# Optimization experiments

Measured on AMD Instinct MI355X. Metric: run time of the kernel, lower is better.

## Reference

```python
import jax, jax.numpy as jnp
import numpy as np

NUM_EXPERTS = 16
HIDDEN_DIM = 1024
TOP_K = 4
INPUT_DIM = 4096
OUTPUT_DIM = 4096
BATCH = 4096


def setup_inputs() -> dict:
    key = jax.random.key(0)
    ks = jax.random.split(key, 6)
    total_cols = NUM_EXPERTS * HIDDEN_DIM
    return {
        "x": jax.random.normal(ks[0], (BATCH, INPUT_DIM), dtype=jnp.float32),
        "gate_w": jax.random.normal(ks[1], (INPUT_DIM, NUM_EXPERTS), dtype=jnp.float32) * 0.02,
        "gate_b": jnp.zeros((NUM_EXPERTS,), dtype=jnp.float32),
        "weight": jax.random.normal(ks[2], (INPUT_DIM, total_cols), dtype=jnp.float32) * 0.01,
        "agg_w": jax.random.normal(ks[3], (total_cols, OUTPUT_DIM), dtype=jnp.float32) * 0.02,
        "agg_b": jnp.zeros((OUTPUT_DIM,), dtype=jnp.float32),
    }


def reference(x, gate_w, gate_b, weight, agg_w, agg_b):
    # 1) gating logits (batch, E), 2) sum over batch -> (E,)
    gating_logits = x @ gate_w + gate_b
    gating_sum = gating_logits.sum(axis=0)
    # 3) global top-k expert selection -> binary mask over experts
    _, topk_inds = jax.lax.top_k(gating_sum, TOP_K)
    expert_mask = jnp.zeros((NUM_EXPERTS,), dtype=x.dtype).at[topk_inds].set(1.0)
    # 4/5) block-sparse matmul: mask replicated over all row blocks, so each
    # expert's column block [e*H:(e+1)*H] is x @ W_block if selected else 0.
    out_sparse = x @ weight  # (batch, E*H)
    col_mask = jnp.repeat(expert_mask, HIDDEN_DIM)  # (E*H,)
    out_sparse = out_sparse * col_mask[None, :]
    # 6) aggregator
    final_out = out_sparse @ agg_w + agg_b
    return final_out
```

## Files before the change

kernel.cpp:

```cpp
#include <hip/hip_runtime.h>
#include <hip/hip_bf16.h>


#define BATCH 4096
#define DIN 4096
#define DOUTD 4096
#define NE 16
#define HD 1024
#define TOPK 4
#define TOTC (NE * HD)
#define NT 64

using bf16 = __hip_bfloat16;
typedef __attribute__((ext_vector_type(8))) short short8;
typedef __attribute__((ext_vector_type(4))) float f32x4;

__device__ inline short f2bs(float f) {
  __hip_bfloat16 h = __float2bfloat16(f);
  return *reinterpret_cast<short*>(&h);
}

__global__ void k_pcol(const float* __restrict__ x, float* __restrict__ pcol) {
  int c = blockIdx.x * 256 + threadIdx.x;
  int r0 = blockIdx.y * 128;
  float s = 0.f;
  for (int r = r0; r < r0 + 128; ++r) s += x[(size_t)r * DIN + c];
  pcol[(size_t)blockIdx.y * DIN + c] = s;
}

__global__ void k_red(const float* __restrict__ pcol, float* __restrict__ colsum) {
  int c = blockIdx.x * 256 + threadIdx.x;
  float s = 0.f;
  for (int j = 0; j < 32; ++j) s += pcol[(size_t)j * DIN + c];
  colsum[c] = s;
}

__global__ void k_gate(const float* __restrict__ colsum, const float* __restrict__ gw,
                       const float* __restrict__ gb, int* __restrict__ ids) {
  __shared__ float red[4][16];
  __shared__ float gs[16];
  int t = threadIdx.x;
  int e = t & 15, kg = t >> 4;
  float p = 0.f;
  for (int k = kg; k < DIN; k += 16) p += colsum[k] * gw[(size_t)k * NE + e];
  p += __shfl_down(p, 32);
  p += __shfl_down(p, 16);
  if ((t & 63) < 16) red[t >> 6][e] = p;
  __syncthreads();
  if (t < 16) gs[t] = red[0][t] + red[1][t] + red[2][t] + red[3][t] + (float)BATCH * gb[t];
  __syncthreads();
  if (t == 0) {
    float v[16];
    #pragma unroll
    for (int i = 0; i < 16; ++i) v[i] = gs[i];
    for (int j = 0; j < TOPK; ++j) {
      int bi = 0;
      float bv = v[0];
      for (int i2 = 1; i2 < 16; ++i2) {
        if (v[i2] > bv) { bv = v[i2]; bi = i2; }
      }
      ids[j] = bi;
      v[bi] = -3.4e38f;
    }
  }
}

__global__ void k_cvt_x(const float* __restrict__ x, bf16* __restrict__ xb) {
  size_t i = ((size_t)blockIdx.x * 256 + threadIdx.x) * 8;
  float4 v0 = *reinterpret_cast<const float4*>(x + i);
  float4 v1 = *reinterpret_cast<const float4*>(x + i + 4);
  short8 r;
  r[0] = f2bs(v0.x); r[1] = f2bs(v0.y); r[2] = f2bs(v0.z); r[3] = f2bs(v0.w);
  r[4] = f2bs(v1.x); r[5] = f2bs(v1.y); r[6] = f2bs(v1.z); r[7] = f2bs(v1.w);
  *reinterpret_cast<short8*>(reinterpret_cast<char*>(xb) + i * 2) = r;
}

__global__ void k_gather_w(const float* __restrict__ w, const int* __restrict__ ids,
                           bf16* __restrict__ wbt) {
  __shared__ float tile[32][33];
  int bid = blockIdx.x;
  int k0 = (bid & 127) * 32, n0 = (bid >> 7) * 32;
  int t = threadIdx.x;
  int tx = t & 31, ty = t >> 5;
  int e = ids[n0 >> 10];
  size_t wcol = (size_t)e * HD + (n0 & 1023) + tx;
  #pragma unroll
  for (int j = 0; j < 4; ++j) {
    int k = k0 + ty + j * 8;
    tile[ty + j * 8][tx] = w[(size_t)k * TOTC + wcol];
  }
  __syncthreads();
  #pragma unroll
  for (int j = 0; j < 4; ++j) {
    int n = n0 + ty + j * 8;
    wbt[(size_t)n * DIN + k0 + tx] = __float2bfloat16(tile[tx][ty + j * 8]);
  }
}

__global__ void k_gather_a(const float* __restrict__ a, const int* __restrict__ ids,
                           bf16* __restrict__ abt) {
  __shared__ float tile[32][33];
  int bid = blockIdx.x;
  int k0 = (bid & 127) * 32, n0 = (bid >> 7) * 32;
  int t = threadIdx.x;
  int tx = t & 31, ty = t >> 5;
  int e = ids[k0 >> 10];
  #pragma unroll
  for (int j = 0; j < 4; ++j) {
    int k = k0 + ty + j * 8;
    size_t ar = (size_t)e * HD + (k & 1023);
    tile[ty + j * 8][tx] = a[ar * DOUTD + n0 + tx];
  }
  __syncthreads();
  #pragma unroll
  for (int j = 0; j < 4; ++j) {
    int n = n0 + ty + j * 8;
    abt[(size_t)n * DIN + k0 + tx] = __float2bfloat16(tile[tx][ty + j * 8]);
  }
}

#define MFMA_BF16 __builtin_amdgcn_mfma_f32_16x16x32_bf16

#define MFMA16(MF0)                                                             \
  __builtin_amdgcn_s_setprio(1);                                               \
  _Pragma("unroll") for (int nf = 0; nf < 4; ++nf) {                            \
    acc[MF0][nf] = MFMA_BF16(aA0, bfrag[nf][0], acc[MF0][nf], 0, 0, 0);         \
    acc[MF0][nf] = MFMA_BF16(aA1, bfrag[nf][1], acc[MF0][nf], 0, 0, 0);         \
    acc[MF0 + 1][nf] = MFMA_BF16(aB0, bfrag[nf][0], acc[MF0 + 1][nf], 0, 0, 0); \
    acc[MF0 + 1][nf] = MFMA_BF16(aB1, bfrag[nf][1], acc[MF0 + 1][nf], 0, 0, 0); \
  }                                                                             \
  __builtin_amdgcn_s_setprio(0);

template <int STORE_F32>
__global__ __launch_bounds__(512, 2) void k_gemm8(
    const bf16* __restrict__ A, const bf16* __restrict__ Bt,
    bf16* __restrict__ Cb, float* __restrict__ Cf, const float* __restrict__ bias) {
  __shared__ __align__(16) char smraw[131072];
  const int t = threadIdx.x;
  const int lane = t & 63;
  const int w = t >> 6;
  const int wr = w >> 2;
  const int wc = w & 3;

  const int bid = blockIdx.x;
  const int swz = (bid & 7) * 32 + (bid >> 3);
  const int bm = (swz >> 4) * 256;
  const int bn = (swz & 15) * 256;

  f32x4 acc[8][4] = {};
  short8 bfrag[4][2];

  const int srow = w * 16 + (lane >> 3);
  const int sgr = lane & 7;

  auto STAGE_A = [&](int buf, int half, int kt) {
    char* lb = smraw + buf * 65536 + half * 16384 + w * 2048 + lane * 16;
    #pragma unroll
    for (int i = 0; i < 2; ++i) {
      int r = srow + i * 8;
      const bf16* g = A + (size_t)(bm + half * 128 + r) * 4096 + kt * 64 + ((sgr ^ (r & 7)) * 8);
      __builtin_amdgcn_global_load_lds(
          (const __attribute__((address_space(1))) void*)g,
          (__attribute__((address_space(3))) void*)(lb + i * 1024), 16, 0, 0);
    }
  };
  auto STAGE_B = [&](int buf, int half, int kt) {
    char* lb = smraw + buf * 65536 + 32768 + half * 16384 + w * 2048 + lane * 16;
    #pragma unroll
    for (int i = 0; i < 2; ++i) {
      int r = srow + i * 8;
      const bf16* g = Bt + (size_t)(bn + half * 128 + r) * 4096 + kt * 64 + ((sgr ^ (r & 7)) * 8);
      __builtin_amdgcn_global_load_lds(
          (const __attribute__((address_space(1))) void*)g,
          (__attribute__((address_space(3))) void*)(lb + i * 1024), 16, 0, 0);
    }
  };
  auto LDA = [&](int buf, int mf, int kk) -> short8 {
    int r = mf * 16 + (lane & 15);
    int kb = ((kk * 4 + (lane >> 4)) ^ (r & 7)) * 16;
    return *reinterpret_cast<const short8*>(smraw + buf * 65536 + wr * 16384 + r * 128 + kb);
  };
  auto LDB = [&](int buf, int nf, int kk) -> short8 {
    int nc = wc * 64 + nf * 16 + (lane & 15);
    int half = nc >> 7, r = nc & 127;
    int kb = ((kk * 4 + (lane >> 4)) ^ (r & 7)) * 16;
    return *reinterpret_cast<const short8*>(smraw + buf * 65536 + 32768 + half * 16384 + r * 128 + kb);
  };

  STAGE_B(0, 0, 0); STAGE_B(0, 1, 0);
  STAGE_A(0, 0, 0); STAGE_A(0, 1, 0);
  STAGE_B(1, 0, 1); STAGE_B(1, 1, 1);
  asm volatile("s_waitcnt vmcnt(4)" ::: "memory");
  __builtin_amdgcn_s_barrier();

  for (int j = 0; j < NT; ++j) {
    const int cur = j & 1, nxt = cur ^ 1;
    {
      #pragma unroll
      for (int nf = 0; nf < 4; ++nf) {
        bfrag[nf][0] = LDB(cur, nf, 0);
        bfrag[nf][1] = LDB(cur, nf, 1);
      }
      short8 aA0 = LDA(cur, 0, 0), aA1 = LDA(cur, 0, 1);
      short8 aB0 = LDA(cur, 1, 0), aB1 = LDA(cur, 1, 1);
      if (j + 1 < NT) STAGE_A(nxt, 0, j + 1);
      __builtin_amdgcn_s_barrier();
      MFMA16(0)
      __builtin_amdgcn_s_barrier();
    }
    {
      short8 aA0 = LDA(cur, 2, 0), aA1 = LDA(cur, 2, 1);
      short8 aB0 = LDA(cur, 3, 0), aB1 = LDA(cur, 3, 1);
      if (j + 1 < NT) STAGE_A(nxt, 1, j + 1);
      __builtin_amdgcn_s_barrier();
      MFMA16(2)
      __builtin_amdgcn_s_barrier();
    }
    {
      short8 aA0 = LDA(cur, 4, 0), aA1 = LDA(cur, 4, 1);
      short8 aB0 = LDA(cur, 5, 0), aB1 = LDA(cur, 5, 1);
      if (j + 2 < NT) STAGE_B(cur, 0, j + 2);
      __builtin_amdgcn_s_barrier();
      MFMA16(4)
      __builtin_amdgcn_s_barrier();
    }
    {
      short8 aA0 = LDA(cur, 6, 0), aA1 = LDA(cur, 6, 1);
      short8 aB0 = LDA(cur, 7, 0), aB1 = LDA(cur, 7, 1);
      if (j + 2 < NT) STAGE_B(cur, 1, j + 2);
      if (j < NT - 2) {
        asm volatile("s_waitcnt vmcnt(4)" ::: "memory");
      } else {
        asm volatile("s_waitcnt vmcnt(0)" ::: "memory");
      }
      __builtin_amdgcn_s_barrier();
      MFMA16(6)
      __builtin_amdgcn_s_barrier();
    }
  }

  const int cr = (lane >> 4) * 4;
  const int cc = lane & 15;
  #pragma unroll
  for (int mf = 0; mf < 8; ++mf) {
    #pragma unroll
    for (int nf = 0; nf < 4; ++nf) {
      int row = bm + wr * 128 + mf * 16 + cr;
      int col = bn + wc * 64 + nf * 16 + cc;
      #pragma unroll
      for (int r = 0; r < 4; ++r) {
        if constexpr (STORE_F32) {
          Cf[(size_t)(row + r) * 4096 + col] = acc[mf][nf][r] + bias[col];
        } else {
          Cb[(size_t)(row + r) * 4096 + col] = __float2bfloat16(acc[mf][nf][r]);
        }
      }
    }
  }
}

extern "C" void kernel_launch(void* const* d_in, const int* in_sizes, int n_in,
                              void* d_out, int out_size, void* d_ws, size_t ws_size,
                              hipStream_t stream) {
  const float* x = (const float*)d_in[0];
  const float* gate_w = (const float*)d_in[1];
  const float* gate_b = (const float*)d_in[2];
  const float* weight = (const float*)d_in[3];
  const float* agg_w = (const float*)d_in[4];
  const float* agg_b = (const float*)d_in[5];
  float* out = (float*)d_out;
  char* ws = (char*)d_ws;

  float* pcol = (float*)ws;
  float* colsum = (float*)(ws + 524288);
  int* ids = (int*)(ws + 540672);
  bf16* mid = (bf16*)(ws + (1u << 20));
  bf16* abt = (bf16*)(ws + (1u << 20) + (32u << 20));
  bf16* xb = (bf16*)d_out;
  bf16* wbt = (bf16*)((char*)d_out + (32u << 20));

  k_pcol<<<dim3(16, 32), 256, 0, stream>>>(x, pcol);
  k_red<<<16, 256, 0, stream>>>(pcol, colsum);
  k_gate<<<1, 256, 0, stream>>>(colsum, gate_w, gate_b, ids);
  k_cvt_x<<<8192, 256, 0, stream>>>(x, xb);
  k_gather_w<<<16384, 256, 0, stream>>>(weight, ids, wbt);
  k_gemm8<0><<<256, 512, 0, stream>>>(xb, wbt, mid, nullptr, nullptr);
  k_gather_a<<<16384, 256, 0, stream>>>(agg_w, ids, abt);
  k_gemm8<1><<<256, 512, 0, stream>>>(mid, abt, nullptr, out, agg_b);
}
```

Before: 410.6 us.

## Fuse x bf16 conversion with column sums, widen gather tiles, unroll GEMM loop

Merges the x-to-bf16 conversion into the column-sum kernel so x is read once, using float4 loads and four partial rows per block. The weight and aggregator gather-transpose kernels move to 64x64 tiles with float4 loads and 16-byte bf16 stores, which cuts the block count and the number of narrow memory transactions. The GEMM main loop is fully unrolled by two k-tiles with compile-time buffer indices, which removes the per-iteration branches on the staging conditions. The wider partial-sum array needs a larger reduction in k_red and a new workspace layout.

```diff
diff --git a/kernel.cpp b/kernel.cpp
--- a/kernel.cpp
+++ b/kernel.cpp
@@ -4,7 +4,6 @@
 
 #define BATCH 4096
 #define DIN 4096
-#define DOUTD 4096
 #define NE 16
 #define HD 1024
 #define TOPK 4
@@ -20,18 +19,29 @@
   return *reinterpret_cast<short*>(&h);
 }
 
-__global__ void k_pcol(const float* __restrict__ x, float* __restrict__ pcol) {
-  int c = blockIdx.x * 256 + threadIdx.x;
-  int r0 = blockIdx.y * 128;
-  float s = 0.f;
-  for (int r = r0; r < r0 + 128; ++r) s += x[(size_t)r * DIN + c];
-  pcol[(size_t)blockIdx.y * DIN + c] = s;
+__global__ void k_cvtsum(const float* __restrict__ x, bf16* __restrict__ xb,
+                         float* __restrict__ pcol) {
+  const int lane = threadIdx.x & 63;
+  const int w = threadIdx.x >> 6;
+  const int c = blockIdx.x * 256 + lane * 4;
+  const int r0 = blockIdx.y * 128 + w * 32;
+  float4 s = {0.f, 0.f, 0.f, 0.f};
+  for (int i = 0; i < 32; ++i) {
+    size_t off = (size_t)(r0 + i) * DIN + c;
+    float4 v = *reinterpret_cast<const float4*>(x + off);
+    s.x += v.x; s.y += v.y; s.z += v.z; s.w += v.w;
+    ushort4 b;
+    b.x = (unsigned short)f2bs(v.x); b.y = (unsigned short)f2bs(v.y);
+    b.z = (unsigned short)f2bs(v.z); b.w = (unsigned short)f2bs(v.w);
+    *reinterpret_cast<ushort4*>(reinterpret_cast<char*>(xb) + off * 2) = b;
+  }
+  *reinterpret_cast<float4*>(pcol + (size_t)(blockIdx.y * 4 + w) * DIN + c) = s;
 }
 
 __global__ void k_red(const float* __restrict__ pcol, float* __restrict__ colsum) {
   int c = blockIdx.x * 256 + threadIdx.x;
   float s = 0.f;
-  for (int j = 0; j < 32; ++j) s += pcol[(size_t)j * DIN + c];
+  for (int j = 0; j < 128; ++j) s += pcol[(size_t)j * DIN + c];
   colsum[c] = s;
 }
 
@@ -56,80 +66,98 @@
     for (int j = 0; j < TOPK; ++j) {
       int bi = 0;
       float bv = v[0];
-      for (int i2 = 1; i2 < 16; ++i2) {
+      for (int i2 = 1; i2 < 16; ++i2)
         if (v[i2] > bv) { bv = v[i2]; bi = i2; }
-      }
       ids[j] = bi;
       v[bi] = -3.4e38f;
     }
   }
 }
 
-__global__ void k_cvt_x(const float* __restrict__ x, bf16* __restrict__ xb) {
-  size_t i = ((size_t)blockIdx.x * 256 + threadIdx.x) * 8;
-  float4 v0 = *reinterpret_cast<const float4*>(x + i);
-  float4 v1 = *reinterpret_cast<const float4*>(x + i + 4);
-  short8 r;
-  r[0] = f2bs(v0.x); r[1] = f2bs(v0.y); r[2] = f2bs(v0.z); r[3] = f2bs(v0.w);
-  r[4] = f2bs(v1.x); r[5] = f2bs(v1.y); r[6] = f2bs(v1.z); r[7] = f2bs(v1.w);
-  *reinterpret_cast<short8*>(reinterpret_cast<char*>(xb) + i * 2) = r;
-}
-
 __global__ void k_gather_w(const float* __restrict__ w, const int* __restrict__ ids,
                            bf16* __restrict__ wbt) {
-  __shared__ float tile[32][33];
-  int bid = blockIdx.x;
-  int k0 = (bid & 127) * 32, n0 = (bid >> 7) * 32;
-  int t = threadIdx.x;
-  int tx = t & 31, ty = t >> 5;
-  int e = ids[n0 >> 10];
-  size_t wcol = (size_t)e * HD + (n0 & 1023) + tx;
+  __shared__ float tile[64 * 65];
+  const int k0 = (blockIdx.x & 63) * 64;
+  const int n0 = (blockIdx.x >> 6) * 64;
+  const int t = threadIdx.x;
+  const int e = ids[n0 >> 10];
+  const int wc0 = e * HD + (n0 & 1023);
+  const int tc = t & 15, kr = t >> 4;
   #pragma unroll
   for (int j = 0; j < 4; ++j) {
-    int k = k0 + ty + j * 8;
-    tile[ty + j * 8][tx] = w[(size_t)k * TOTC + wcol];
-  }
-  __syncthreads();
-  #pragma unroll
-  for (int j = 0; j < 4; ++j) {
-    int n = n0 + ty + j * 8;
-    wbt[(size_t)n * DIN + k0 + tx] = __float2bfloat16(tile[tx][ty + j * 8]);
+    int kk = kr + j * 16;
+    float4 v = *reinterpret_cast<const float4*>(w + (size_t)(k0 + kk) * TOTC + wc0 + tc * 4);
+    float* dst = &tile[kk * 65 + tc * 4];
+    dst[0] = v.x; dst[1] = v.y; dst[2] = v.z; dst[3] = v.w;
+  }
+  __syncthreads();
+  const int tk = t & 7, nr0 = t >> 3;
+  #pragma unroll
+  for (int i = 0; i < 2; ++i) {
+    int n = n0 + nr0 + i * 32;
+    short8 r;
+    #pragma unroll
+    for (int m = 0; m < 8; ++m) r[m] = f2bs(tile[(tk * 8 + m) * 65 + nr0 + i * 32]);
+    *reinterpret_cast<short8*>(wbt + (size_t)n * DIN + k0 + tk * 8) = r;
   }
 }
 
 __global__ void k_gather_a(const float* __restrict__ a, const int* __restrict__ ids,
                            bf16* __restrict__ abt) {
-  __shared__ float tile[32][33];
-  int bid = blockIdx.x;
-  int k0 = (bid & 127) * 32, n0 = (bid >> 7) * 32;
-  int t = threadIdx.x;
-  int tx = t & 31, ty = t >> 5;
-  int e = ids[k0 >> 10];
+  __shared__ float tile[64 * 65];
+  const int k0 = (blockIdx.x & 63) * 64;
+  const int n0 = (blockIdx.x >> 6) * 64;
+  const int t = threadIdx.x;
+  const int e = ids[k0 >> 10];
+  const int ar0 = e * HD + (k0 & 1023);
+  const int tc = t & 15, kr = t >> 4;
   #pragma unroll
   for (int j = 0; j < 4; ++j) {
-    int k = k0 + ty + j * 8;
-    size_t ar = (size_t)e * HD + (k & 1023);
-    tile[ty + j * 8][tx] = a[ar * DOUTD + n0 + tx];
-  }
-  __syncthreads();
-  #pragma unroll
-  for (int j = 0; j < 4; ++j) {
-    int n = n0 + ty + j * 8;
-    abt[(size_t)n * DIN + k0 + tx] = __float2bfloat16(tile[tx][ty + j * 8]);
+    int kk = kr + j * 16;
+    float4 v = *reinterpret_cast<const float4*>(a + (size_t)(ar0 + kk) * 4096 + n0 + tc * 4);
+    float* dst = &tile[kk * 65 + tc * 4];
+    dst[0] = v.x; dst[1] = v.y; dst[2] = v.z; dst[3] = v.w;
+  }
+  __syncthreads();
+  const int tk = t & 7, nr0 = t >> 3;
+  #pragma unroll
+  for (int i = 0; i < 2; ++i) {
+    int n = n0 + nr0 + i * 32;
+    short8 r;
+    #pragma unroll
+    for (int m = 0; m < 8; ++m) r[m] = f2bs(tile[(tk * 8 + m) * 65 + nr0 + i * 32]);
+    *reinterpret_cast<short8*>(abt + (size_t)n * DIN + k0 + tk * 8) = r;
   }
 }
 
 #define MFMA_BF16 __builtin_amdgcn_mfma_f32_16x16x32_bf16
-
-#define MFMA16(MF0)                                                             \
-  __builtin_amdgcn_s_setprio(1);                                               \
-  _Pragma("unroll") for (int nf = 0; nf < 4; ++nf) {                            \
-    acc[MF0][nf] = MFMA_BF16(aA0, bfrag[nf][0], acc[MF0][nf], 0, 0, 0);         \
-    acc[MF0][nf] = MFMA_BF16(aA1, bfrag[nf][1], acc[MF0][nf], 0, 0, 0);         \
-    acc[MF0 + 1][nf] = MFMA_BF16(aB0, bfrag[nf][0], acc[MF0 + 1][nf], 0, 0, 0); \
-    acc[MF0 + 1][nf] = MFMA_BF16(aB1, bfrag[nf][1], acc[MF0 + 1][nf], 0, 0, 0); \
-  }                                                                             \
-  __builtin_amdgcn_s_setprio(0);
+#define VM4 asm volatile("s_waitcnt vmcnt(4)" ::: "memory")
+#define VM0 asm volatile("s_waitcnt vmcnt(0)" ::: "memory")
+#define NOST ((void)0)
+
+#define PH(BUF, Q, STG, GATE)                                                   \
+  do {                                                                          \
+    if ((Q) == 0) {                                                             \
+      _Pragma("unroll") for (int nf = 0; nf < 4; ++nf) {                        \
+        bfrag[nf][0] = LDB(BUF, nf, 0);                                         \
+        bfrag[nf][1] = LDB(BUF, nf, 1);                                         \
+      }                                                                         \
+    }                                                                           \
+    short8 aA0 = LDA(BUF, 2 * (Q), 0), aA1 = LDA(BUF, 2 * (Q), 1);              \
+    short8 aB0 = LDA(BUF, 2 * (Q) + 1, 0), aB1 = LDA(BUF, 2 * (Q) + 1, 1);      \
+    STG;                                                                        \
+    GATE;                                                                       \
+    __builtin_amdgcn_s_barrier();                                               \
+    __builtin_amdgcn_s_setprio(1);                                              \
+    _Pragma("unroll") for (int nf = 0; nf < 4; ++nf) {                          \
+      acc[2 * (Q)][nf] = MFMA_BF16(aA0, bfrag[nf][0], acc[2 * (Q)][nf], 0, 0, 0);       \
+      acc[2 * (Q)][nf] = MFMA_BF16(aA1, bfrag[nf][1], acc[2 * (Q)][nf], 0, 0, 0);       \
+      acc[2 * (Q) + 1][nf] = MFMA_BF16(aB0, bfrag[nf][0], acc[2 * (Q) + 1][nf], 0, 0, 0); \
+      acc[2 * (Q) + 1][nf] = MFMA_BF16(aB1, bfrag[nf][1], acc[2 * (Q) + 1][nf], 0, 0, 0); \
+    }                                                                           \
+    __builtin_amdgcn_s_setprio(0);                                              \
+    __builtin_amdgcn_s_barrier();                                               \
+  } while (0)
 
 template <int STORE_F32>
 __global__ __launch_bounds__(512, 2) void k_gemm8(
@@ -190,54 +218,28 @@
   STAGE_B(0, 0, 0); STAGE_B(0, 1, 0);
   STAGE_A(0, 0, 0); STAGE_A(0, 1, 0);
   STAGE_B(1, 0, 1); STAGE_B(1, 1, 1);
-  asm volatile("s_waitcnt vmcnt(4)" ::: "memory");
+  VM4;
   __builtin_amdgcn_s_barrier();
 
-  for (int j = 0; j < NT; ++j) {
-    const int cur = j & 1, nxt = cur ^ 1;
-    {
-      #pragma unroll
-      for (int nf = 0; nf < 4; ++nf) {
-        bfrag[nf][0] = LDB(cur, nf, 0);
-        bfrag[nf][1] = LDB(cur, nf, 1);
-      }
-      short8 aA0 = LDA(cur, 0, 0), aA1 = LDA(cur, 0, 1);
-      short8 aB0 = LDA(cur, 1, 0), aB1 = LDA(cur, 1, 1);
-      if (j + 1 < NT) STAGE_A(nxt, 0, j + 1);
-      __builtin_amdgcn_s_barrier();
-      MFMA16(0)
-      __builtin_amdgcn_s_barrier();
-    }
-    {
-      short8 aA0 = LDA(cur, 2, 0), aA1 = LDA(cur, 2, 1);
-      short8 aB0 = LDA(cur, 3, 0), aB1 = LDA(cur, 3, 1);
-      if (j + 1 < NT) STAGE_A(nxt, 1, j + 1);
-      __builtin_amdgcn_s_barrier();
-      MFMA16(2)
-      __builtin_amdgcn_s_barrier();
-    }
-    {
-      short8 aA0 = LDA(cur, 4, 0), aA1 = LDA(cur, 4, 1);
-      short8 aB0 = LDA(cur, 5, 0), aB1 = LDA(cur, 5, 1);
-      if (j + 2 < NT) STAGE_B(cur, 0, j + 2);
-      __builtin_amdgcn_s_barrier();
-      MFMA16(4)
-      __builtin_amdgcn_s_barrier();
-    }
-    {
-      short8 aA0 = LDA(cur, 6, 0), aA1 = LDA(cur, 6, 1);
-      short8 aB0 = LDA(cur, 7, 0), aB1 = LDA(cur, 7, 1);
-      if (j + 2 < NT) STAGE_B(cur, 1, j + 2);
-      if (j < NT - 2) {
-        asm volatile("s_waitcnt vmcnt(4)" ::: "memory");
-      } else {
-        asm volatile("s_waitcnt vmcnt(0)" ::: "memory");
-      }
-      __builtin_amdgcn_s_barrier();
-      MFMA16(6)
-      __builtin_amdgcn_s_barrier();
-    }
-  }
+  for (int tt = 0; tt < 31; ++tt) {
+    const int a = 2 * tt;
+    PH(0, 0, STAGE_A(1, 0, a + 1), NOST);
+    PH(0, 1, STAGE_A(1, 1, a + 1), NOST);
+    PH(0, 2, STAGE_B(0, 0, a + 2), NOST);
+    PH(0, 3, STAGE_B(0, 1, a + 2), VM4);
+    PH(1, 0, STAGE_A(0, 0, a + 2), NOST);
+    PH(1, 1, STAGE_A(0, 1, a + 2), NOST);
+    PH(1, 2, STAGE_B(1, 0, a + 3), NOST);
+    PH(1, 3, STAGE_B(1, 1, a + 3), VM4);
+  }
+  PH(0, 0, STAGE_A(1, 0, 63), NOST);
+  PH(0, 1, STAGE_A(1, 1, 63), NOST);
+  PH(0, 2, NOST, NOST);
+  PH(0, 3, NOST, VM0);
+  PH(1, 0, NOST, NOST);
+  PH(1, 1, NOST, NOST);
+  PH(1, 2, NOST, NOST);
+  PH(1, 3, NOST, NOST);
 
   const int cr = (lane >> 4) * 4;
   const int cc = lane & 15;
@@ -272,19 +274,18 @@
   char* ws = (char*)d_ws;
 
   float* pcol = (float*)ws;
-  float* colsum = (float*)(ws + 524288);
-  int* ids = (int*)(ws + 540672);
-  bf16* mid = (bf16*)(ws + (1u << 20));
-  bf16* abt = (bf16*)(ws + (1u << 20) + (32u << 20));
+  float* colsum = (float*)(ws + (2u << 20));
+  int* ids = (int*)(ws + (2u << 20) + 16384);
+  bf16* mid = (bf16*)(ws + (4u << 20));
+  bf16* abt = (bf16*)(ws + (36u << 20));
   bf16* xb = (bf16*)d_out;
   bf16* wbt = (bf16*)((char*)d_out + (32u << 20));
 
-  k_pcol<<<dim3(16, 32), 256, 0, stream>>>(x, pcol);
+  k_cvtsum<<<dim3(16, 32), 256, 0, stream>>>(x, xb, pcol);
   k_red<<<16, 256, 0, stream>>>(pcol, colsum);
   k_gate<<<1, 256, 0, stream>>>(colsum, gate_w, gate_b, ids);
-  k_cvt_x<<<8192, 256, 0, stream>>>(x, xb);
-  k_gather_w<<<16384, 256, 0, stream>>>(weight, ids, wbt);
+  k_gather_w<<<4096, 256, 0, stream>>>(weight, ids, wbt);
   k_gemm8<0><<<256, 512, 0, stream>>>(xb, wbt, mid, nullptr, nullptr);
-  k_gather_a<<<16384, 256, 0, stream>>>(agg_w, ids, abt);
+  k_gather_a<<<4096, 256, 0, stream>>>(agg_w, ids, abt);
   k_gemm8<1><<<256, 512, 0, stream>>>(mid, abt, nullptr, out, agg_b);
 }
```

Result: faster. 385.5 us (-6.1%).
